# Optimization experiments

Measured on AMD Instinct MI355X. Metric: run time of the kernel, lower is better.

The kernel has to match this reference:

```python
import jax, jax.numpy as jnp
import numpy as np

N_HEAD = 16
SCALE = float(np.sqrt(1024 // N_HEAD))  # source multiplies by sqrt(head_dim) (faithful to bug)


def setup_inputs() -> dict:
    key = jax.random.key(0)
    ks = jax.random.split(key, 4)
    B, T, D = 4, 2048, 1024
    std = 1.0 / np.sqrt(D)
    return {
        "x": jax.random.normal(ks[0], (B, T, D), dtype=jnp.float32),
        "Wq": jax.random.normal(ks[1], (D, D), dtype=jnp.float32) * std,
        "bq": jnp.zeros((D,), dtype=jnp.float32),
        "Wk": jax.random.normal(ks[2], (D, D), dtype=jnp.float32) * std,
        "bk": jnp.zeros((D,), dtype=jnp.float32),
        "Wv": jax.random.normal(ks[3], (D, D), dtype=jnp.float32) * std,
        "bv": jnp.zeros((D,), dtype=jnp.float32),
    }


def reference(x, Wq, bq, Wk, bk, Wv, bv):
    B, T, D = x.shape
    H = N_HEAD
    hd = D // H
    # linear projections (torch Linear: x @ W^T + b)
    q = x @ Wq.T + bq
    k = x @ Wk.T + bk
    v = x @ Wv.T + bv
    # [B, H, T, hd]
    q = q.reshape(B, T, H, hd).transpose(0, 2, 1, 3)
    k = k.reshape(B, T, H, hd).transpose(0, 2, 1, 3)
    v = v.reshape(B, T, H, hd).transpose(0, 2, 1, 3)
    # scores [B, H, T, T]; note: source MULTIPLIES by sqrt(head_dim)
    att = jnp.einsum("bhqd,bhkd->bhqk", q, k) * SCALE
    causal = jnp.tril(jnp.ones((T, T), dtype=bool))
    att = jnp.where(causal, att, -jnp.inf)
    att = jax.nn.softmax(att, axis=-1)
    y = jnp.einsum("bhqk,bhkd->bhqd", att, v)
    return y.transpose(0, 2, 1, 3).reshape(B, T, D)
```

## Files before the change

### kernel.cpp

```cpp
#include <hip/hip_runtime.h>
#include <math.h>

#define TSEQ   2048
#define NBATCH 4
#define NHEAD  16
#define HDIM   64
#define DMODEL 1024
#define MROWS  (NBATCH * TSEQ)
#define QSCALE 11.541560327111707f

typedef float f32x4  __attribute__((ext_vector_type(4)));
typedef short bf16x8 __attribute__((ext_vector_type(8)));
typedef _Float16 f16x8 __attribute__((ext_vector_type(8)));

static __device__ __forceinline__ short f2bf(float f) {
    union { float f; unsigned u; } a; a.f = f;
    unsigned r = a.u + 0x7FFFu + ((a.u >> 16) & 1u);
    return (short)(r >> 16);
}
static __device__ __forceinline__ float bf2f(short s) {
    union { unsigned u; float f; } a; a.u = ((unsigned)(unsigned short)s) << 16;
    return a.f;
}
static __device__ __forceinline__ unsigned pkh(float a, float b) {
    union { _Float16 h[2]; unsigned u; } z;
    z.h[0] = (_Float16)a; z.h[1] = (_Float16)b;
    return z.u;
}

static __device__ __forceinline__ void async_copy16(void* lds, const void* g) {
    __builtin_amdgcn_global_load_lds(
        (const __attribute__((address_space(1))) void*)g,
        (__attribute__((address_space(3))) void*)lds, 16, 0, 0);
}

#define X_F4 (MROWS * DMODEL / 4)
#define W_F4 (DMODEL * DMODEL / 4)
__global__ __launch_bounds__(256) void split_all(
    const float* __restrict__ x,
    const float* __restrict__ wq, const float* __restrict__ wk,
    const float* __restrict__ wv,
    short* __restrict__ Xhi, short* __restrict__ Xlo,
    short* __restrict__ Whi, short* __restrict__ Wlo)
{
    int gid = blockIdx.x * 256 + threadIdx.x;
    const float* src; short* dh; short* dl; int off;
    if (gid < X_F4) {
        src = x; dh = Xhi; dl = Xlo; off = gid;
    } else {
        int r = gid - X_F4;
        int z = r >> 18;
        off = r & (W_F4 - 1);
        src = (z == 0) ? wq : (z == 1) ? wk : wv;
        dh = Whi + (size_t)z * DMODEL * DMODEL;
        dl = Wlo + (size_t)z * DMODEL * DMODEL;
    }
    float4 v = ((const float4*)src)[off];
    float f[4] = {v.x, v.y, v.z, v.w};
    short h[4], l[4];
    #pragma unroll
    for (int c = 0; c < 4; c++) {
        h[c] = f2bf(f[c]);
        l[c] = f2bf(f[c] - bf2f(h[c]));
    }
    *(float2*)(dh + (size_t)off * 4) = *(const float2*)h;
    *(float2*)(dl + (size_t)off * 4) = *(const float2*)l;
}

__global__ __launch_bounds__(256, 2) void qkv_gemm_mfma(
    const short* __restrict__ Xhi, const short* __restrict__ Xlo,
    const short* __restrict__ Wh3, const short* __restrict__ Wl3,
    const float* __restrict__ bq, const float* __restrict__ bk,
    const float* __restrict__ bv,
    short* __restrict__ Qhi, short* __restrict__ Qlo,
    short* __restrict__ Khi, short* __restrict__ Klo,
    _Float16* __restrict__ VgT)
{
    const int z = blockIdx.z;
    const bool dolo = (z != 2);
    const short* Wh = Wh3 + (size_t)z * DMODEL * DMODEL;
    const short* Wl = Wl3 + (size_t)z * DMODEL * DMODEL;
    const float* bias = (z == 0) ? bq : (z == 1) ? bk : bv;

    __shared__ __align__(16) short Ah[128 * 32];
    __shared__ __align__(16) short Al[128 * 32];
    __shared__ __align__(16) short Bh[128 * 32];
    __shared__ __align__(16) short Bl[128 * 32];

    const int tid  = threadIdx.x;
    const int w    = tid >> 6;
    const int lane = tid & 63;
    const int t    = lane & 15;
    const int quad = lane >> 4;
    const int wm   = w >> 1, wn = w & 1;

    const int orig = blockIdx.x + (blockIdx.y << 3);
    const int nw   = (orig & 7) * 64 + (orig >> 3);
    const int bm   = (nw >> 3) * 128;
    const int bn   = (nw & 7) * 128;

    const int r_local = lane >> 2;
    const int kq      = (lane & 3) ^ ((r_local >> 1) & 3);
    const int row0    = w * 32 + r_local;
    const int slotq   = (quad ^ ((t >> 1) & 3)) * 8;

    f32x4 acc[4][4];
    #pragma unroll
    for (int i = 0; i < 4; i++)
        #pragma unroll
        for (int j = 0; j < 4; j++) acc[i][j] = (f32x4){0.f, 0.f, 0.f, 0.f};

    for (int k0 = 0; k0 < DMODEL; k0 += 32) {
        __syncthreads();
        #pragma unroll
        for (int i = 0; i < 2; i++) {
            int row = row0 + i * 16;
            size_t ga = (size_t)(bm + row) * DMODEL + k0 + kq * 8;
            size_t gb = (size_t)(bn + row) * DMODEL + k0 + kq * 8;
            int ldst = (w * 32 + i * 16) * 32;
            async_copy16(&Ah[ldst], Xhi + ga);
            async_copy16(&Bh[ldst], Wh + gb);
            if (dolo) {
                async_copy16(&Al[ldst], Xlo + ga);
                async_copy16(&Bl[ldst], Wl + gb);
            }
        }
        __syncthreads();

        bf16x8 ah[4], al[4], bh[4], bl[4];
        #pragma unroll
        for (int mt = 0; mt < 4; mt++) {
            int off = (wm * 64 + mt * 16 + t) * 32 + slotq;
            ah[mt] = *(const bf16x8*)&Ah[off];
            if (dolo) al[mt] = *(const bf16x8*)&Al[off];
        }
        #pragma unroll
        for (int nt = 0; nt < 4; nt++) {
            int off = (wn * 64 + nt * 16 + t) * 32 + slotq;
            bh[nt] = *(const bf16x8*)&Bh[off];
            if (dolo) bl[nt] = *(const bf16x8*)&Bl[off];
        }
        #pragma unroll
        for (int mt = 0; mt < 4; mt++)
            #pragma unroll
            for (int nt = 0; nt < 4; nt++) {
                if (dolo) {
                    acc[mt][nt] = __builtin_amdgcn_mfma_f32_16x16x32_bf16(
                        al[mt], bh[nt], acc[mt][nt], 0, 0, 0);
                    acc[mt][nt] = __builtin_amdgcn_mfma_f32_16x16x32_bf16(
                        ah[mt], bl[nt], acc[mt][nt], 0, 0, 0);
                }
                acc[mt][nt] = __builtin_amdgcn_mfma_f32_16x16x32_bf16(
                    ah[mt], bh[nt], acc[mt][nt], 0, 0, 0);
            }
    }

    const float scale = (z == 0) ? QSCALE : 1.0f;
    const int n_base = bn + wn * 64;
    const int h_head = n_base >> 6;
    float bvs[4];
    #pragma unroll
    for (int nt = 0; nt < 4; nt++)
        bvs[nt] = bias[n_base + nt * 16 + t];

    #pragma unroll
    for (int mt = 0; mt < 4; mt++) {
        #pragma unroll
        for (int r = 0; r < 4; r++) {
            int m  = bm + wm * 64 + mt * 16 + quad * 4 + r;
            int b_ = m >> 11;
            int t_ = m & 2047;
            #pragma unroll
            for (int nt = 0; nt < 4; nt++) {
                int d = nt * 16 + t;
                float v = (acc[mt][nt][r] + bvs[nt]) * scale;
                if (z == 2) {
                    size_t idx = ((size_t)(b_ * NHEAD + h_head) * HDIM + d) * TSEQ + t_;
                    VgT[idx] = (_Float16)v;
                } else {
                    size_t idx = (((size_t)(b_ * NHEAD + h_head) * TSEQ + t_) << 6) + d;
                    short hb = f2bf(v);
                    short lb = f2bf(v - bf2f(hb));
                    if (z == 0) { Qhi[idx] = hb; Qlo[idx] = lb; }
                    else        { Khi[idx] = hb; Klo[idx] = lb; }
                }
            }
        }
    }
}

__global__ __launch_bounds__(256, 2) void attn_fwd(
    const short* __restrict__ Qhi, const short* __restrict__ Qlo,
    const short* __restrict__ Khi, const short* __restrict__ Klo,
    const _Float16* __restrict__ VgT,
    float* __restrict__ out)
{
    __shared__ __align__(16) short    Kh_lds[2][64 * 64];
    __shared__ __align__(16) short    Kl_lds[2][64 * 64];
    __shared__ __align__(16) _Float16 Vt_lds[2][64 * 64];

    const int tid  = threadIdx.x;

    const int orig = blockIdx.x + (blockIdx.y << 3);
    const int nw   = (orig & 7) * 64 + (orig >> 3);
    const int bh   = nw >> 3;
    const int xt   = nw & 7;

    const int b    = bh >> 4, h = bh & 15;
    const int w    = tid >> 6;
    const int lane = tid & 63;
    const int t    = lane & 15;
    const int quad = lane >> 4;

    const int rl      = w * 8 + (lane >> 3);
    const int chsw    = (lane & 7) ^ ((lane >> 3) & 7);
    const int ld_off  = (w * 8) * 64;

    const size_t kbase = (size_t)bh * TSEQ;
    const size_t vbase = (size_t)bh * HDIM;

    const int rs0 = ((0 * 4 + quad) ^ (t & 7)) * 8;
    const int rs1 = ((1 * 4 + quad) ^ (t & 7)) * 8;
    const int qsw = ((quad & 1) << 1) | (quad >> 1);
    const int rp0 = ((0 * 4 + qsw) ^ (t & 7)) * 8;
    const int rp1 = ((1 * 4 + qsw) ^ (t & 7)) * 8;
    const bool hi4 = (quad & 1);

    f16x8 ones;
    #pragma unroll
    for (int i = 0; i < 8; i++) ones[i] = (_Float16)1.0f;

    auto stage = [&](int kt, int bf) {
        #pragma unroll
        for (int i = 0; i < 2; i++) {
            int row = i * 32 + rl;
            const short* gk = Khi + (kbase + kt * 64 + row) * 64 + chsw * 8;
            async_copy16(&Kh_lds[bf][(i * 32) * 64 + ld_off], gk);
            const short* gl = Klo + (kbase + kt * 64 + row) * 64 + chsw * 8;
            async_copy16(&Kl_lds[bf][(i * 32) * 64 + ld_off], gl);
            const _Float16* gv = VgT + (vbase + row) * TSEQ + kt * 64 + chsw * 8;
            async_copy16(&Vt_lds[bf][(i * 32) * 64 + ld_off], gv);
        }
    };

    #pragma unroll 1
    for (int seg = 0; seg < 2; seg++) {
        const int qb = seg ? (15 - xt) : xt;

        bf16x8 qh[2][2], ql[2][2];
        #pragma unroll
        for (int mt = 0; mt < 2; mt++) {
            size_t qrow = kbase + qb * 128 + w * 32 + mt * 16 + t;
            #pragma unroll
            for (int dh = 0; dh < 2; dh++) {
                qh[mt][dh] = *(const bf16x8*)(Qhi + qrow * 64 + dh * 32 + quad * 8);
                ql[mt][dh] = *(const bf16x8*)(Qlo + qrow * 64 + dh * 32 + quad * 8);
            }
        }

        f32x4 O[2][4], Ol[2];
        #pragma unroll
        for (int mt = 0; mt < 2; mt++) {
            Ol[mt] = (f32x4){0.f, 0.f, 0.f, 0.f};
            #pragma unroll
            for (int j = 0; j < 4; j++) O[mt][j] = (f32x4){0.f, 0.f, 0.f, 0.f};
        }
        float m_st[2];
        m_st[0] = -1e30f; m_st[1] = -1e30f;

        const int npair = qb + 1;

        #pragma unroll 1
        for (int p = 0; p < npair; p++) {
            __syncthreads();
            stage(2 * p, 0);
            stage(2 * p + 1, 1);
            __syncthreads();

            #pragma unroll
            for (int mt = 0; mt < 2; mt++) {
                f32x4 S[8];
                __builtin_amdgcn_s_setprio(1);
                #pragma unroll
                for (int c8 = 0; c8 < 8; c8++) {
                    S[c8] = (f32x4){0.f, 0.f, 0.f, 0.f};
                    const int bf = c8 >> 2;
                    const int rowoff = ((c8 & 3) * 16 + t) * 64;
                    {
                        bf16x8 kh = *(const bf16x8*)&Kh_lds[bf][rowoff + rs0];
                        bf16x8 kl = *(const bf16x8*)&Kl_lds[bf][rowoff + rs0];
                        S[c8] = __builtin_amdgcn_mfma_f32_16x16x32_bf16(kh, ql[mt][0], S[c8], 0, 0, 0);
                        S[c8] = __builtin_amdgcn_mfma_f32_16x16x32_bf16(kl, qh[mt][0], S[c8], 0, 0, 0);
                        S[c8] = __builtin_amdgcn_mfma_f32_16x16x32_bf16(kh, qh[mt][0], S[c8], 0, 0, 0);
                    }
                    {
                        bf16x8 kh = *(const bf16x8*)&Kh_lds[bf][rowoff + rs1];
                        bf16x8 kl = *(const bf16x8*)&Kl_lds[bf][rowoff + rs1];
                        S[c8] = __builtin_amdgcn_mfma_f32_16x16x32_bf16(kh, ql[mt][1], S[c8], 0, 0, 0);
                        S[c8] = __builtin_amdgcn_mfma_f32_16x16x32_bf16(kl, qh[mt][1], S[c8], 0, 0, 0);
                        S[c8] = __builtin_amdgcn_mfma_f32_16x16x32_bf16(kh, qh[mt][1], S[c8], 0, 0, 0);
                    }
                }
                __builtin_amdgcn_s_setprio(0);

                if (p == qb) {
                    const int qloc = w * 32 + mt * 16 + t;
                    #pragma unroll
                    for (int c8 = 0; c8 < 8; c8++) {
                        int kp = c8 * 16 + quad * 4;
                        #pragma unroll
                        for (int r = 0; r < 4; r++)
                            if (kp + r > qloc) S[c8][r] = -1e30f;
                    }
                }

                float mx = S[0][0];
                #pragma unroll
                for (int c8 = 0; c8 < 8; c8++)
                    #pragma unroll
                    for (int r = 0; r < 4; r++)
                        mx = fmaxf(mx, S[c8][r]);
                mx = fmaxf(mx, __shfl_xor(mx, 16));
                mx = fmaxf(mx, __shfl_xor(mx, 32));

                bool need = mx > m_st[mt] + 8.0f;
                if (__ballot(need)) {
                    float mn = fmaxf(m_st[mt], mx);
                    float al = exp2f(m_st[mt] - mn);
                    m_st[mt] = mn;
                    #pragma unroll
                    for (int r = 0; r < 4; r++) {
                        float a = __shfl(al, (lane & 48) + quad * 4 + r);
                        Ol[mt][r] *= a;
                        #pragma unroll
                        for (int ct2 = 0; ct2 < 4; ct2++) O[mt][ct2][r] *= a;
                    }
                }

                #pragma unroll
                for (int c8 = 0; c8 < 8; c8++)
                    #pragma unroll
                    for (int r = 0; r < 4; r++)
                        S[c8][r] = exp2f(S[c8][r] - m_st[mt]);

                unsigned P2[8][2];
                #pragma unroll
                for (int c8 = 0; c8 < 8; c8++) {
                    P2[c8][0] = pkh(S[c8][0], S[c8][1]);
                    P2[c8][1] = pkh(S[c8][2], S[c8][3]);
                }

                unsigned FR[4][4];
                #pragma unroll
                for (int tau = 0; tau < 4; tau++) {
                    #pragma unroll
                    for (int rp = 0; rp < 2; rp++) {
                        unsigned X  = P2[2 * tau][rp];
                        unsigned Y  = P2[2 * tau + 1][rp];
                        unsigned Xs = (unsigned)__shfl_xor((int)X, 16);
                        unsigned Ys = (unsigned)__shfl_xor((int)Y, 16);
                        FR[tau][rp]     = hi4 ? Ys : X;
                        FR[tau][2 + rp] = hi4 ? Y  : Xs;
                    }
                }

                #pragma unroll
                for (int tau = 0; tau < 4; tau++) {
                    union { unsigned u[4]; f16x8 v; } pu;
                    pu.u[0] = FR[tau][0]; pu.u[1] = FR[tau][1];
                    pu.u[2] = FR[tau][2]; pu.u[3] = FR[tau][3];
                    f16x8 pf = pu.v;
                    const int bf  = tau >> 1;
                    const int rsP = (tau & 1) ? rp1 : rp0;
                    __builtin_amdgcn_s_setprio(1);
                    #pragma unroll
                    for (int ct2 = 0; ct2 < 4; ct2++) {
                        f16x8 v = *(const f16x8*)&Vt_lds[bf][(ct2 * 16 + t) * 64 + rsP];
                        O[mt][ct2] = __builtin_amdgcn_mfma_f32_16x16x32_f16(pf, v, O[mt][ct2], 0, 0, 0);
                    }
                    Ol[mt] = __builtin_amdgcn_mfma_f32_16x16x32_f16(pf, ones, Ol[mt], 0, 0, 0);
                    __builtin_amdgcn_s_setprio(0);
                }
            }
        }

        #pragma unroll
        for (int mt = 0; mt < 2; mt++) {
            float* ob = out + ((size_t)b * TSEQ + qb * 128 + w * 32 + mt * 16 + quad * 4) * DMODEL
                      + h * 64;
            #pragma unroll
            for (int r = 0; r < 4; r++) {
                float inv = 1.0f / Ol[mt][r];
                #pragma unroll
                for (int ct2 = 0; ct2 < 4; ct2++)
                    ob[(size_t)r * DMODEL + ct2 * 16 + t] = O[mt][ct2][r] * inv;
            }
        }
    }
}

extern "C" void kernel_launch(void* const* d_in, const int* in_sizes, int n_in,
                              void* d_out, int out_size, void* d_ws, size_t ws_size,
                              hipStream_t stream)
{
    const float* x  = (const float*)d_in[0];
    const float* Wq = (const float*)d_in[1];
    const float* bq = (const float*)d_in[2];
    const float* Wk = (const float*)d_in[3];
    const float* bk = (const float*)d_in[4];
    const float* Wv = (const float*)d_in[5];
    const float* bv = (const float*)d_in[6];

    const size_t TEN = (size_t)MROWS * DMODEL;
    const size_t WEN = (size_t)DMODEL * DMODEL;
    short* Xhi = (short*)d_ws;
    short* Xlo = Xhi + TEN;
    short* Whi = Xlo + TEN;
    short* Wlo = Whi + 3 * WEN;
    short* Qhi = Wlo + 3 * WEN;
    short* Qlo = Qhi + TEN;
    short* Khi = Qlo + TEN;
    short* Klo = Khi + TEN;
    _Float16* VgT = (_Float16*)(Klo + TEN);
    float* out = (float*)d_out;

    int nsplit = (X_F4 + 3 * W_F4) / 256;
    split_all<<<nsplit, 256, 0, stream>>>(x, Wq, Wk, Wv, Xhi, Xlo, Whi, Wlo);

    dim3 gg(DMODEL / 128, MROWS / 128, 3);
    qkv_gemm_mfma<<<gg, 256, 0, stream>>>(Xhi, Xlo, Whi, Wlo, bq, bk, bv,
                                          Qhi, Qlo, Khi, Klo, VgT);

    dim3 ga(8, NBATCH * NHEAD);
    attn_fwd<<<ga, 256, 0, stream>>>(Qhi, Qlo, Khi, Klo, VgT, out);
}
```

Measured before the change: 349.8 us.

## Double-buffer K/V tiles with async prefetch across the key loop

Replaces the per-pair load-then-compute loop, which used two full syncs per 128 keys, with a single-tile loop over 64-key tiles. The next-but-one tile is prefetched asynchronously into the buffer just consumed, and waitcnt throttling keeps one tile in flight. The goal is to hide global-to-LDS load latency behind the MFMA work. In exchange, the online-softmax max, rescale and shuffle steps run twice as often, each over half as many keys, and there are more barriers per key.

```diff
diff --git a/kernel.cpp b/kernel.cpp
--- a/kernel.cpp
+++ b/kernel.cpp
@@ -230,7 +230,7 @@
     #pragma unroll
     for (int i = 0; i < 8; i++) ones[i] = (_Float16)1.0f;
 
-    auto stage = [&](int kt, int bf) {
+    auto stage_tile = [&](int kt, int bf) {
         #pragma unroll
         for (int i = 0; i < 2; i++) {
             int row = i * 32 + rl;
@@ -246,6 +246,7 @@
     #pragma unroll 1
     for (int seg = 0; seg < 2; seg++) {
         const int qb = seg ? (15 - xt) : xt;
+        const int NT = 2 * (qb + 1);
 
         bf16x8 qh[2][2], ql[2][2];
         #pragma unroll
@@ -268,24 +269,24 @@
         float m_st[2];
         m_st[0] = -1e30f; m_st[1] = -1e30f;
 
-        const int npair = qb + 1;
+        stage_tile(0, 0);
+        stage_tile(1, 1);
+        asm volatile("s_waitcnt vmcnt(6)" ::: "memory");
+        __builtin_amdgcn_s_barrier();
 
         #pragma unroll 1
-        for (int p = 0; p < npair; p++) {
-            __syncthreads();
-            stage(2 * p, 0);
-            stage(2 * p + 1, 1);
-            __syncthreads();
+        for (int kt = 0; kt < NT; kt++) {
+            const int bf = kt & 1;
+            const int dk = kt - 2 * qb;
 
             #pragma unroll
             for (int mt = 0; mt < 2; mt++) {
-                f32x4 S[8];
+                f32x4 S[4];
                 __builtin_amdgcn_s_setprio(1);
                 #pragma unroll
-                for (int c8 = 0; c8 < 8; c8++) {
+                for (int c8 = 0; c8 < 4; c8++) {
                     S[c8] = (f32x4){0.f, 0.f, 0.f, 0.f};
-                    const int bf = c8 >> 2;
-                    const int rowoff = ((c8 & 3) * 16 + t) * 64;
+                    const int rowoff = (c8 * 16 + t) * 64;
                     {
                         bf16x8 kh = *(const bf16x8*)&Kh_lds[bf][rowoff + rs0];
                         bf16x8 kl = *(const bf16x8*)&Kl_lds[bf][rowoff + rs0];
@@ -303,11 +304,11 @@
                 }
                 __builtin_amdgcn_s_setprio(0);
 
-                if (p == qb) {
+                if (dk >= 0) {
                     const int qloc = w * 32 + mt * 16 + t;
                     #pragma unroll
-                    for (int c8 = 0; c8 < 8; c8++) {
-                        int kp = c8 * 16 + quad * 4;
+                    for (int c8 = 0; c8 < 4; c8++) {
+                        int kp = dk * 64 + c8 * 16 + quad * 4;
                         #pragma unroll
                         for (int r = 0; r < 4; r++)
                             if (kp + r > qloc) S[c8][r] = -1e30f;
@@ -316,7 +317,7 @@
 
                 float mx = S[0][0];
                 #pragma unroll
-                for (int c8 = 0; c8 < 8; c8++)
+                for (int c8 = 0; c8 < 4; c8++)
                     #pragma unroll
                     for (int r = 0; r < 4; r++)
                         mx = fmaxf(mx, S[c8][r]);
@@ -338,21 +339,21 @@
                 }
 
                 #pragma unroll
-                for (int c8 = 0; c8 < 8; c8++)
+                for (int c8 = 0; c8 < 4; c8++)
                     #pragma unroll
                     for (int r = 0; r < 4; r++)
                         S[c8][r] = exp2f(S[c8][r] - m_st[mt]);
 
-                unsigned P2[8][2];
-                #pragma unroll
-                for (int c8 = 0; c8 < 8; c8++) {
+                unsigned P2[4][2];
+                #pragma unroll
+                for (int c8 = 0; c8 < 4; c8++) {
                     P2[c8][0] = pkh(S[c8][0], S[c8][1]);
                     P2[c8][1] = pkh(S[c8][2], S[c8][3]);
                 }
 
-                unsigned FR[4][4];
-                #pragma unroll
-                for (int tau = 0; tau < 4; tau++) {
+                unsigned FR[2][4];
+                #pragma unroll
+                for (int tau = 0; tau < 2; tau++) {
                     #pragma unroll
                     for (int rp = 0; rp < 2; rp++) {
                         unsigned X  = P2[2 * tau][rp];
@@ -365,13 +366,12 @@
                 }
 
                 #pragma unroll
-                for (int tau = 0; tau < 4; tau++) {
+                for (int tau = 0; tau < 2; tau++) {
                     union { unsigned u[4]; f16x8 v; } pu;
                     pu.u[0] = FR[tau][0]; pu.u[1] = FR[tau][1];
                     pu.u[2] = FR[tau][2]; pu.u[3] = FR[tau][3];
                     f16x8 pf = pu.v;
-                    const int bf  = tau >> 1;
-                    const int rsP = (tau & 1) ? rp1 : rp0;
+                    const int rsP = tau ? rp1 : rp0;
                     __builtin_amdgcn_s_setprio(1);
                     #pragma unroll
                     for (int ct2 = 0; ct2 < 4; ct2++) {
@@ -382,6 +382,15 @@
                     __builtin_amdgcn_s_setprio(0);
                 }
             }
+
+            __builtin_amdgcn_s_barrier();
+            if (kt + 2 < NT) {
+                stage_tile(kt + 2, bf);
+                asm volatile("s_waitcnt vmcnt(6)" ::: "memory");
+            } else {
+                asm volatile("s_waitcnt vmcnt(0)" ::: "memory");
+            }
+            __builtin_amdgcn_s_barrier();
         }
 
         #pragma unroll
```

After: 352.0 us. No clear change (+0.6%).

## Enlarge QKV GEMM tiles to 256x256 with double-buffered, phased MFMA pipeline

Applied to the files above, without the earlier changes.

The QKV projection GEMM now uses 512-thread blocks computing 256x256 tiles, double-buffered in LDS. Loads for the next k-steps are issued between four phased MFMA sub-blocks, with explicit waitcnt, barriers and s_setprio. Block-to-tile mapping is remapped for XCD locality. The aim is more data reuse per LDS load and overlap of global loads with MFMA work. The cost is higher register pressure (acc[8][4] with launch_bounds(512,2)), more LDS and fewer blocks.

```diff
diff --git a/kernel.cpp b/kernel.cpp
--- a/kernel.cpp
+++ b/kernel.cpp
@@ -67,7 +67,9 @@
     *(float2*)(dl + (size_t)off * 4) = *(const float2*)l;
 }
 
-__global__ __launch_bounds__(256, 2) void qkv_gemm_mfma(
+#define PLANE(d, p) ((((d) << 2) + (p)) * (256 * 32))
+
+__global__ __launch_bounds__(512, 2) void qkv_gemm_mfma(
     const short* __restrict__ Xhi, const short* __restrict__ Xlo,
     const short* __restrict__ Wh3, const short* __restrict__ Wl3,
     const float* __restrict__ bq, const float* __restrict__ bk,
@@ -82,81 +84,164 @@
     const short* Wl = Wl3 + (size_t)z * DMODEL * DMODEL;
     const float* bias = (z == 0) ? bq : (z == 1) ? bk : bv;
 
-    __shared__ __align__(16) short Ah[128 * 32];
-    __shared__ __align__(16) short Al[128 * 32];
-    __shared__ __align__(16) short Bh[128 * 32];
-    __shared__ __align__(16) short Bl[128 * 32];
+    __shared__ __align__(16) short LDSM[2 * 4 * 256 * 32];
 
     const int tid  = threadIdx.x;
     const int w    = tid >> 6;
     const int lane = tid & 63;
     const int t    = lane & 15;
     const int quad = lane >> 4;
-    const int wm   = w >> 1, wn = w & 1;
-
-    const int orig = blockIdx.x + (blockIdx.y << 3);
-    const int nw   = (orig & 7) * 64 + (orig >> 3);
-    const int bm   = (nw >> 3) * 128;
-    const int bn   = (nw & 7) * 128;
+    const int wr   = w >> 2;
+    const int wc   = w & 3;
+
+    const int l   = blockIdx.x + (blockIdx.y << 2);
+    const int xcd = l & 7, idx = l >> 3;
+    const int bn  = (xcd >> 1) * 256;
+    const int bm  = ((xcd & 1) * 16 + idx) * 256;
 
     const int r_local = lane >> 2;
     const int kq      = (lane & 3) ^ ((r_local >> 1) & 3);
     const int row0    = w * 32 + r_local;
     const int slotq   = (quad ^ ((t >> 1) & 3)) * 8;
 
-    f32x4 acc[4][4];
+    f32x4 acc[8][4];
     #pragma unroll
-    for (int i = 0; i < 4; i++)
+    for (int i = 0; i < 8; i++)
         #pragma unroll
         for (int j = 0; j < 4; j++) acc[i][j] = (f32x4){0.f, 0.f, 0.f, 0.f};
 
-    for (int k0 = 0; k0 < DMODEL; k0 += 32) {
-        __syncthreads();
+    auto stage_p0 = [&](int kt, int d) {
         #pragma unroll
         for (int i = 0; i < 2; i++) {
-            int row = row0 + i * 16;
-            size_t ga = (size_t)(bm + row) * DMODEL + k0 + kq * 8;
-            size_t gb = (size_t)(bn + row) * DMODEL + k0 + kq * 8;
+            int row  = row0 + i * 16;
             int ldst = (w * 32 + i * 16) * 32;
-            async_copy16(&Ah[ldst], Xhi + ga);
-            async_copy16(&Bh[ldst], Wh + gb);
-            if (dolo) {
-                async_copy16(&Al[ldst], Xlo + ga);
-                async_copy16(&Bl[ldst], Wl + gb);
-            }
-        }
-        __syncthreads();
-
-        bf16x8 ah[4], al[4], bh[4], bl[4];
+            size_t ga = (size_t)(bm + row) * DMODEL + kt * 32 + kq * 8;
+            size_t gb = (size_t)(bn + row) * DMODEL + kt * 32 + kq * 8;
+            async_copy16(&LDSM[PLANE(d, 0) + ldst], Xhi + ga);
+            async_copy16(&LDSM[PLANE(d, 2) + ldst], Wh + gb);
+        }
+    };
+    auto stage_p1 = [&](int kt, int d) {
+        #pragma unroll
+        for (int i = 0; i < 2; i++) {
+            int row  = row0 + i * 16;
+            int ldst = (w * 32 + i * 16) * 32;
+            size_t ga = (size_t)(bm + row) * DMODEL + kt * 32 + kq * 8;
+            size_t gb = (size_t)(bn + row) * DMODEL + kt * 32 + kq * 8;
+            async_copy16(&LDSM[PLANE(d, 1) + ldst], Xlo + ga);
+            async_copy16(&LDSM[PLANE(d, 3) + ldst], Wl + gb);
+        }
+    };
+
+    const int NT = DMODEL / 32;
+
+    stage_p0(0, 0);
+    if (dolo) stage_p1(0, 0);
+    stage_p0(1, 1);
+    asm volatile("s_waitcnt vmcnt(4)" ::: "memory");
+    __builtin_amdgcn_s_barrier();
+
+    #pragma unroll 1
+    for (int kt = 0; kt < NT; kt++) {
+        const int d = kt & 1;
+        bf16x8 ah[8], al[8], bh[4], bl[4];
+
         #pragma unroll
         for (int mt = 0; mt < 4; mt++) {
-            int off = (wm * 64 + mt * 16 + t) * 32 + slotq;
-            ah[mt] = *(const bf16x8*)&Ah[off];
-            if (dolo) al[mt] = *(const bf16x8*)&Al[off];
-        }
-        #pragma unroll
-        for (int nt = 0; nt < 4; nt++) {
-            int off = (wn * 64 + nt * 16 + t) * 32 + slotq;
-            bh[nt] = *(const bf16x8*)&Bh[off];
-            if (dolo) bl[nt] = *(const bf16x8*)&Bl[off];
-        }
+            int off = (wr * 128 + mt * 16 + t) * 32 + slotq;
+            ah[mt] = *(const bf16x8*)&LDSM[PLANE(d, 0) + off];
+            if (dolo) al[mt] = *(const bf16x8*)&LDSM[PLANE(d, 1) + off];
+        }
+        #pragma unroll
+        for (int nt = 0; nt < 2; nt++) {
+            int off = (wc * 64 + nt * 16 + t) * 32 + slotq;
+            bh[nt] = *(const bf16x8*)&LDSM[PLANE(d, 2) + off];
+            if (dolo) bl[nt] = *(const bf16x8*)&LDSM[PLANE(d, 3) + off];
+        }
+        if (dolo && kt + 1 < NT) stage_p1(kt + 1, d ^ 1);
+        asm volatile("s_waitcnt lgkmcnt(0)" ::: "memory");
+        __builtin_amdgcn_s_barrier();
+        __builtin_amdgcn_s_setprio(1);
         #pragma unroll
         for (int mt = 0; mt < 4; mt++)
             #pragma unroll
-            for (int nt = 0; nt < 4; nt++) {
+            for (int nt = 0; nt < 2; nt++) {
                 if (dolo) {
-                    acc[mt][nt] = __builtin_amdgcn_mfma_f32_16x16x32_bf16(
-                        al[mt], bh[nt], acc[mt][nt], 0, 0, 0);
-                    acc[mt][nt] = __builtin_amdgcn_mfma_f32_16x16x32_bf16(
-                        ah[mt], bl[nt], acc[mt][nt], 0, 0, 0);
-                }
-                acc[mt][nt] = __builtin_amdgcn_mfma_f32_16x16x32_bf16(
-                    ah[mt], bh[nt], acc[mt][nt], 0, 0, 0);
-            }
+                    acc[mt][nt] = __builtin_amdgcn_mfma_f32_16x16x32_bf16(al[mt], bh[nt], acc[mt][nt], 0, 0, 0);
+                    acc[mt][nt] = __builtin_amdgcn_mfma_f32_16x16x32_bf16(ah[mt], bl[nt], acc[mt][nt], 0, 0, 0);
+                }
+                acc[mt][nt] = __builtin_amdgcn_mfma_f32_16x16x32_bf16(ah[mt], bh[nt], acc[mt][nt], 0, 0, 0);
+            }
+        __builtin_amdgcn_s_setprio(0);
+        __builtin_amdgcn_s_barrier();
+
+        #pragma unroll
+        for (int nt = 2; nt < 4; nt++) {
+            int off = (wc * 64 + nt * 16 + t) * 32 + slotq;
+            bh[nt] = *(const bf16x8*)&LDSM[PLANE(d, 2) + off];
+            if (dolo) bl[nt] = *(const bf16x8*)&LDSM[PLANE(d, 3) + off];
+        }
+        asm volatile("s_waitcnt lgkmcnt(0)" ::: "memory");
+        __builtin_amdgcn_s_barrier();
+        __builtin_amdgcn_s_setprio(1);
+        #pragma unroll
+        for (int mt = 0; mt < 4; mt++)
+            #pragma unroll
+            for (int nt = 2; nt < 4; nt++) {
+                if (dolo) {
+                    acc[mt][nt] = __builtin_amdgcn_mfma_f32_16x16x32_bf16(al[mt], bh[nt], acc[mt][nt], 0, 0, 0);
+                    acc[mt][nt] = __builtin_amdgcn_mfma_f32_16x16x32_bf16(ah[mt], bl[nt], acc[mt][nt], 0, 0, 0);
+                }
+                acc[mt][nt] = __builtin_amdgcn_mfma_f32_16x16x32_bf16(ah[mt], bh[nt], acc[mt][nt], 0, 0, 0);
+            }
+        __builtin_amdgcn_s_setprio(0);
+        __builtin_amdgcn_s_barrier();
+
+        #pragma unroll
+        for (int mt = 4; mt < 8; mt++) {
+            int off = (wr * 128 + mt * 16 + t) * 32 + slotq;
+            ah[mt] = *(const bf16x8*)&LDSM[PLANE(d, 0) + off];
+            if (dolo) al[mt] = *(const bf16x8*)&LDSM[PLANE(d, 1) + off];
+        }
+        asm volatile("s_waitcnt lgkmcnt(0)" ::: "memory");
+        __builtin_amdgcn_s_barrier();
+        __builtin_amdgcn_s_setprio(1);
+        #pragma unroll
+        for (int mt = 4; mt < 8; mt++)
+            #pragma unroll
+            for (int nt = 2; nt < 4; nt++) {
+                if (dolo) {
+                    acc[mt][nt] = __builtin_amdgcn_mfma_f32_16x16x32_bf16(al[mt], bh[nt], acc[mt][nt], 0, 0, 0);
+                    acc[mt][nt] = __builtin_amdgcn_mfma_f32_16x16x32_bf16(ah[mt], bl[nt], acc[mt][nt], 0, 0, 0);
+                }
+                acc[mt][nt] = __builtin_amdgcn_mfma_f32_16x16x32_bf16(ah[mt], bh[nt], acc[mt][nt], 0, 0, 0);
+            }
+        __builtin_amdgcn_s_setprio(0);
+        __builtin_amdgcn_s_barrier();
+
+        if (kt + 2 < NT) {
+            stage_p0(kt + 2, d);
+            asm volatile("s_waitcnt vmcnt(4)" ::: "memory");
+        } else {
+            asm volatile("s_waitcnt vmcnt(0)" ::: "memory");
+        }
+        __builtin_amdgcn_s_setprio(1);
+        #pragma unroll
+        for (int mt = 4; mt < 8; mt++)
+            #pragma unroll
+            for (int nt = 0; nt < 2; nt++) {
+                if (dolo) {
+                    acc[mt][nt] = __builtin_amdgcn_mfma_f32_16x16x32_bf16(al[mt], bh[nt], acc[mt][nt], 0, 0, 0);
+                    acc[mt][nt] = __builtin_amdgcn_mfma_f32_16x16x32_bf16(ah[mt], bl[nt], acc[mt][nt], 0, 0, 0);
+                }
+                acc[mt][nt] = __builtin_amdgcn_mfma_f32_16x16x32_bf16(ah[mt], bh[nt], acc[mt][nt], 0, 0, 0);
+            }
+        __builtin_amdgcn_s_setprio(0);
+        __builtin_amdgcn_s_barrier();
     }
 
     const float scale = (z == 0) ? QSCALE : 1.0f;
-    const int n_base = bn + wn * 64;
+    const int n_base = bn + wc * 64;
     const int h_head = n_base >> 6;
     float bvs[4];
     #pragma unroll
@@ -164,10 +249,10 @@
         bvs[nt] = bias[n_base + nt * 16 + t];
 
     #pragma unroll
-    for (int mt = 0; mt < 4; mt++) {
+    for (int mt = 0; mt < 8; mt++) {
         #pragma unroll
         for (int r = 0; r < 4; r++) {
-            int m  = bm + wm * 64 + mt * 16 + quad * 4 + r;
+            int m  = bm + wr * 128 + mt * 16 + quad * 4 + r;
             int b_ = m >> 11;
             int t_ = m & 2047;
             #pragma unroll
@@ -427,8 +512,8 @@
     int nsplit = (X_F4 + 3 * W_F4) / 256;
     split_all<<<nsplit, 256, 0, stream>>>(x, Wq, Wk, Wv, Xhi, Xlo, Whi, Wlo);
 
-    dim3 gg(DMODEL / 128, MROWS / 128, 3);
-    qkv_gemm_mfma<<<gg, 256, 0, stream>>>(Xhi, Xlo, Whi, Wlo, bq, bk, bv,
+    dim3 gg(DMODEL / 256, MROWS / 256, 3);
+    qkv_gemm_mfma<<<gg, 512, 0, stream>>>(Xhi, Xlo, Whi, Wlo, bq, bk, bv,
                                           Qhi, Qlo, Khi, Klo, VgT);
 
     dim3 ga(8, NBATCH * NHEAD);
```

Measured after the change: 379.5 us. 1.09x slower.
